# Optimization experiments

Measured on AMD Instinct MI355X. Metric: run time of the kernel, lower is better.

## Reference

```python
import jax, jax.numpy as jnp
import numpy as np

EPS = 1e-10   # eps added inside cumprod, as in _compute_weights
FAR = 1e10    # last delta, as in forward()
NEAR_D, FAR_D = 2.0, 6.0  # typical NeRF near/far bounds for depth sampling

N_RAYS, N_PTS = 65536, 128


def setup_inputs() -> dict:
    key = jax.random.key(0)
    k1, k2, k3 = jax.random.split(key, 3)
    # densities are non-negative (raw sigma output after relu/softplus)
    density = jax.random.uniform(k1, (N_RAYS, N_PTS), dtype=jnp.float32) * 2.0
    feature = jax.random.uniform(k2, (N_RAYS, N_PTS, 3), dtype=jnp.float32)
    # monotonically increasing sample depths along each ray in [NEAR_D, FAR_D]
    depth_values = jnp.sort(
        jax.random.uniform(k3, (N_RAYS, N_PTS), dtype=jnp.float32,
                           minval=NEAR_D, maxval=FAR_D), axis=-1)
    return {"density": density, "feature": feature, "depth_values": depth_values}


def reference(density, feature, depth_values):
    # deltas: diff of sample depths, last delta = 1e10  -> [N, P]
    deltas = jnp.concatenate(
        [depth_values[..., 1:] - depth_values[..., :-1],
         jnp.full_like(depth_values[..., :1], FAR)], axis=-1)
    alpha = 1.0 - jnp.exp(-deltas * density)                      # [N, P]
    # transmittance: cumprod(1-alpha+eps) rolled right with T[...,0]=1
    Tinc = jnp.cumprod(1.0 - alpha + EPS, axis=-1)                # [N, P]
    T = jnp.concatenate([jnp.ones_like(Tinc[..., :1]), Tinc[..., :-1]], axis=-1)
    weights = T * alpha                                           # [N, P]
    # weighted feature (rgb) and depth aggregation over samples
    rgb = jnp.einsum('np,npc->nc', weights, feature)              # [N, 3]
    depth = jnp.einsum('np,npc->nc', weights,
                       jnp.broadcast_to(depth_values[..., None], feature.shape))  # [N, 3]
    return rgb, depth
```

## Files before the change

### kernel.cpp

```cpp
#include <hip/hip_runtime.h>

#define N_PTS 128
#define EPS_F 1e-10f
#define FAR_F 1e10f

template<int CTRL, int ROW_MASK>
__device__ __forceinline__ float dpp_mov(float src, float old) {
    union { float f; int i; } s, o, r;
    s.f = src; o.f = old;
    r.i = __builtin_amdgcn_update_dpp(o.i, s.i, CTRL, ROW_MASK, 0xF, false);
    return r.f;
}

__device__ __forceinline__ float wave64_reduce_add(float x) {
    x += dpp_mov<0x111, 0xF>(x, 0.0f);
    x += dpp_mov<0x112, 0xF>(x, 0.0f);
    x += dpp_mov<0x114, 0xF>(x, 0.0f);
    x += dpp_mov<0x118, 0xF>(x, 0.0f);
    x += dpp_mov<0x142, 0xA>(x, 0.0f);
    x += dpp_mov<0x143, 0xC>(x, 0.0f);
    return x;
}

__global__ __launch_bounds__(256) void volrend_kernel(
        const float* __restrict__ density,
        const float* __restrict__ feature,
        const float* __restrict__ depth,
        float* __restrict__ out, int n_rays) {
    const int lane = threadIdx.x & 63;
    const int ray  = blockIdx.x * 4 + (threadIdx.x >> 6);
    if (ray >= n_rays) return;

    const float2 dns = ((const float2*)(density + (size_t)ray * N_PTS))[lane];
    const float2 z   = ((const float2*)(depth   + (size_t)ray * N_PTS))[lane];
    const float2* fp = (const float2*)(feature + (size_t)ray * (N_PTS * 3));
    const float2 fa = fp[lane * 3 + 0];
    const float2 fb = fp[lane * 3 + 1];
    const float2 fc = fp[lane * 3 + 2];

    float nz     = dpp_mov<0x130, 0xF>(z.x, 0.0f);
    float delta0 = z.y - z.x;
    float delta1 = (lane == 63) ? FAR_F : (nz - z.y);

    float e0 = __expf(-delta0 * dns.x);
    float e1 = __expf(-delta1 * dns.y);
    float alpha0 = 1.0f - e0;
    float alpha1 = 1.0f - e1;
    float f0 = e0 + EPS_F;
    float f1 = e1 + EPS_F;

    float p = f0 * f1;
    p *= dpp_mov<0x111, 0xF>(p, 1.0f);
    p *= dpp_mov<0x112, 0xF>(p, 1.0f);
    p *= dpp_mov<0x114, 0xF>(p, 1.0f);
    p *= dpp_mov<0x118, 0xF>(p, 1.0f);
    p *= dpp_mov<0x142, 0xA>(p, 1.0f);
    p *= dpp_mov<0x143, 0xC>(p, 1.0f);
    float T0 = dpp_mov<0x138, 0xF>(p, 1.0f);

    float w0 = T0 * alpha0;
    float T1 = T0 * f0;
    float w1 = T1 * alpha1;

    float rx = wave64_reduce_add(w0 * fa.x + w1 * fb.y);
    float ry = wave64_reduce_add(w0 * fa.y + w1 * fc.x);
    float rz = wave64_reduce_add(w0 * fb.x + w1 * fc.y);
    float dd = wave64_reduce_add(w0 * z.x  + w1 * z.y);

    if (lane == 63) {
        float* o  = out + (size_t)ray * 3;
        o[0] = rx; o[1] = ry; o[2] = rz;
        float* od = out + (size_t)n_rays * 3 + (size_t)ray * 3;
        od[0] = dd; od[1] = dd; od[2] = dd;
    }
}

extern "C" void kernel_launch(void* const* d_in, const int* in_sizes, int n_in,
                              void* d_out, int out_size, void* d_ws, size_t ws_size,
                              hipStream_t stream) {
    const float* density = (const float*)d_in[0];
    const float* feature = (const float*)d_in[1];
    const float* depth   = (const float*)d_in[2];
    float* out = (float*)d_out;
    const int n_rays = in_sizes[0] / N_PTS;
    const int blocks = (n_rays + 3) / 4;
    volrend_kernel<<<blocks, 256, 0, stream>>>(density, feature, depth, out, n_rays);
}
```

Before: 187.9 us.

## Map two rays per wave with float4 loads and half-wave scans

Each wave now processes two rays, one per 32-lane half, and each lane handles four samples loaded as float4 instead of two as float2. The scan and reductions drop the final cross-row DPP step so they stay within each half-wave, and T0 is forced to 1 at the first lane of each half. The goal is wider memory transactions, fewer DPP/reduction instructions per ray and more per-lane work, at the cost of more registers. The bounds check on ray was removed, so it relies on n_rays being a multiple of eight.

```diff
diff --git a/kernel.cpp b/kernel.cpp
--- a/kernel.cpp
+++ b/kernel.cpp
@@ -12,13 +12,12 @@
     return r.f;
 }
 
-__device__ __forceinline__ float wave64_reduce_add(float x) {
+__device__ __forceinline__ float half32_reduce_add(float x) {
     x += dpp_mov<0x111, 0xF>(x, 0.0f);
     x += dpp_mov<0x112, 0xF>(x, 0.0f);
     x += dpp_mov<0x114, 0xF>(x, 0.0f);
     x += dpp_mov<0x118, 0xF>(x, 0.0f);
     x += dpp_mov<0x142, 0xA>(x, 0.0f);
-    x += dpp_mov<0x143, 0xC>(x, 0.0f);
     return x;
 }
 
@@ -28,46 +27,48 @@
         const float* __restrict__ depth,
         float* __restrict__ out, int n_rays) {
     const int lane = threadIdx.x & 63;
-    const int ray  = blockIdx.x * 4 + (threadIdx.x >> 6);
-    if (ray >= n_rays) return;
+    const int hl   = lane & 31;
+    const int wave = (blockIdx.x * 256 + threadIdx.x) >> 6;
+    const int ray  = wave * 2 + (lane >> 5);
 
-    const float2 dns = ((const float2*)(density + (size_t)ray * N_PTS))[lane];
-    const float2 z   = ((const float2*)(depth   + (size_t)ray * N_PTS))[lane];
-    const float2* fp = (const float2*)(feature + (size_t)ray * (N_PTS * 3));
-    const float2 fa = fp[lane * 3 + 0];
-    const float2 fb = fp[lane * 3 + 1];
-    const float2 fc = fp[lane * 3 + 2];
+    const float4 dns = ((const float4*)(density + (size_t)ray * N_PTS))[hl];
+    const float4 z   = ((const float4*)(depth   + (size_t)ray * N_PTS))[hl];
+    const float4* fp = (const float4*)(feature + (size_t)ray * (N_PTS * 3));
+    const float4 fa = fp[hl * 3 + 0];
+    const float4 fb = fp[hl * 3 + 1];
+    const float4 fc = fp[hl * 3 + 2];
 
-    float nz     = dpp_mov<0x130, 0xF>(z.x, 0.0f);
-    float delta0 = z.y - z.x;
-    float delta1 = (lane == 63) ? FAR_F : (nz - z.y);
+    float nz = dpp_mov<0x130, 0xF>(z.x, 0.0f);
+    float d0 = z.y - z.x;
+    float d1 = z.z - z.y;
+    float d2 = z.w - z.z;
+    float d3 = (hl == 31) ? FAR_F : (nz - z.w);
 
-    float e0 = __expf(-delta0 * dns.x);
-    float e1 = __expf(-delta1 * dns.y);
-    float alpha0 = 1.0f - e0;
-    float alpha1 = 1.0f - e1;
-    float f0 = e0 + EPS_F;
-    float f1 = e1 + EPS_F;
+    float e0 = __expf(-d0 * dns.x), e1 = __expf(-d1 * dns.y);
+    float e2 = __expf(-d2 * dns.z), e3 = __expf(-d3 * dns.w);
+    float f0 = e0 + EPS_F, f1 = e1 + EPS_F, f2 = e2 + EPS_F, f3 = e3 + EPS_F;
+    float a0 = 1.0f - e0,  a1 = 1.0f - e1,  a2 = 1.0f - e2,  a3 = 1.0f - e3;
 
-    float p = f0 * f1;
+    float p = (f0 * f1) * (f2 * f3);
     p *= dpp_mov<0x111, 0xF>(p, 1.0f);
     p *= dpp_mov<0x112, 0xF>(p, 1.0f);
     p *= dpp_mov<0x114, 0xF>(p, 1.0f);
     p *= dpp_mov<0x118, 0xF>(p, 1.0f);
     p *= dpp_mov<0x142, 0xA>(p, 1.0f);
-    p *= dpp_mov<0x143, 0xC>(p, 1.0f);
     float T0 = dpp_mov<0x138, 0xF>(p, 1.0f);
+    T0 = (hl == 0) ? 1.0f : T0;
 
-    float w0 = T0 * alpha0;
-    float T1 = T0 * f0;
-    float w1 = T1 * alpha1;
+    float w0 = T0 * a0; float T1 = T0 * f0;
+    float w1 = T1 * a1; float T2 = T1 * f1;
+    float w2 = T2 * a2; float T3 = T2 * f2;
+    float w3 = T3 * a3;
 
-    float rx = wave64_reduce_add(w0 * fa.x + w1 * fb.y);
-    float ry = wave64_reduce_add(w0 * fa.y + w1 * fc.x);
-    float rz = wave64_reduce_add(w0 * fb.x + w1 * fc.y);
-    float dd = wave64_reduce_add(w0 * z.x  + w1 * z.y);
+    float rx = half32_reduce_add(w0 * fa.x + w1 * fa.w + w2 * fb.z + w3 * fc.y);
+    float ry = half32_reduce_add(w0 * fa.y + w1 * fb.x + w2 * fb.w + w3 * fc.z);
+    float rz = half32_reduce_add(w0 * fa.z + w1 * fb.y + w2 * fc.x + w3 * fc.w);
+    float dd = half32_reduce_add(w0 * z.x  + w1 * z.y  + w2 * z.z  + w3 * z.w);
 
-    if (lane == 63) {
+    if (hl == 31) {
         float* o  = out + (size_t)ray * 3;
         o[0] = rx; o[1] = ry; o[2] = rz;
         float* od = out + (size_t)n_rays * 3 + (size_t)ray * 3;
@@ -83,6 +84,6 @@
     const float* depth   = (const float*)d_in[2];
     float* out = (float*)d_out;
     const int n_rays = in_sizes[0] / N_PTS;
-    const int blocks = (n_rays + 3) / 4;
+    const int blocks = (n_rays + 7) / 8;
     volrend_kernel<<<blocks, 256, 0, stream>>>(density, feature, depth, out, n_rays);
 }
```

Result: no change. 191.2 us (+1.7%).
